# Performance work log

Hardware: AMD Instinct MI355X
Metric: run time of the kernel (lower is better)

The kernel has to match this reference:

```python
import jax, jax.numpy as jnp
import numpy as np

N_NODES = 10000
N_EDGES = 160000
N_GRAPHS = 64
X_IN = 128
HID = 64
EDGE_DIM = 16
HEADS = 4
# (in_dim, out_dim_per_head) for the 3 TransformerConv layers (concat=False)
DIMS = [(X_IN, HID), (HID, 2 * HID), (2 * HID, HID)]
WNAMES = [f"{n}{l}" for l in (1, 2, 3) for n in ("wq", "bq", "wk", "bk", "wv", "bv", "we", "ws", "bs")]


def setup_inputs() -> dict:
    key = jax.random.key(0)
    ks = iter(jax.random.split(key, 64))
    inp = {}
    inp["x"] = jax.random.normal(next(ks), (N_NODES, X_IN), jnp.float32)
    inp["edge_index"] = jax.random.randint(next(ks), (2, N_EDGES), 0, N_NODES)
    inp["edge_attr"] = jax.random.normal(next(ks), (N_EDGES, EDGE_DIM), jnp.float32)
    inp["batch"] = jnp.sort(jax.random.randint(next(ks), (N_NODES,), 0, N_GRAPHS))
    for l, (din, dout) in enumerate(DIMS, 1):
        hd = HEADS * dout
        for nm, shape in [("wq", (din, hd)), ("wk", (din, hd)), ("wv", (din, hd)),
                          ("we", (EDGE_DIM, hd)), ("ws", (din, dout))]:
            inp[f"{nm}{l}"] = jax.random.normal(next(ks), shape, jnp.float32) * 0.05
        inp[f"bq{l}"] = jnp.zeros((hd,), jnp.float32)
        inp[f"bk{l}"] = jnp.zeros((hd,), jnp.float32)
        inp[f"bv{l}"] = jnp.zeros((hd,), jnp.float32)
        inp[f"bs{l}"] = jnp.zeros((dout,), jnp.float32)
    return inp


def _transformer_conv(x, src, dst, edge_attr, wq, bq, wk, bk, wv, bv, we, ws, bs, dout):
    """PyG TransformerConv, concat=False, root_weight=True, with edge features."""
    N = x.shape[0]
    q = (x @ wq + bq).reshape(N, HEADS, dout)
    k = (x @ wk + bk).reshape(N, HEADS, dout)
    v = (x @ wv + bv).reshape(N, HEADS, dout)
    e = (edge_attr @ we).reshape(-1, HEADS, dout)  # [E, H, C]
    k_j = k[src] + e                               # edge-conditioned keys
    alpha = jnp.einsum("ehd,ehd->eh", q[dst], k_j) * (1.0 / float(dout) ** 0.5)  # [E, H]
    # numerically stable segment softmax over incoming edges of each dst node
    a_max = jax.ops.segment_max(alpha, dst, num_segments=N)
    ex = jnp.exp(alpha - a_max[dst])
    den = jax.ops.segment_sum(ex, dst, num_segments=N)
    attn = ex / den[dst]
    agg = jax.ops.segment_sum((v[src] + e) * attn[..., None], dst, num_segments=N)  # [N, H, C]
    return agg.mean(axis=1) + x @ ws + bs  # concat=False -> head mean; + skip


def _forward(x, edge_attr, edge_index, batch, params):
    src, dst = edge_index[0], edge_index[1]
    h = x
    for l, (_, dout) in enumerate(DIMS, 1):
        p = [params[f"{n}{l}"] for n in ("wq", "bq", "wk", "bk", "wv", "bv", "we", "ws", "bs")]
        h = jax.nn.elu(_transformer_conv(h, src, dst, edge_attr, *p, dout))
    # global mean pool over graphs
    s = jax.ops.segment_sum(h, batch, num_segments=N_GRAPHS)
    cnt = jax.ops.segment_sum(jnp.ones((h.shape[0], 1), h.dtype), batch, num_segments=N_GRAPHS)
    return s / jnp.maximum(cnt, 1.0)


def reference(x, edge_index, edge_attr, batch,
              wq1, bq1, wk1, bk1, wv1, bv1, we1, ws1, bs1,
              wq2, bq2, wk2, bk2, wv2, bv2, we2, ws2, bs2,
              wq3, bq3, wk3, bk3, wv3, bv3, we3, ws3, bs3):
    params = dict(locals())
    return _forward(x, edge_attr, edge_index, batch, params)
```

## Files before the change

kernel.cpp:

```cpp
#include <hip/hip_runtime.h>
#include <hip/hip_fp16.h>
#include <math.h>

#define N_NODES 10000
#define N_EDGES 160000
#define N_GRAPHS 64

using half8 = __attribute__((ext_vector_type(8))) _Float16;
using floatx4 = __attribute__((ext_vector_type(4))) float;
using h2v = __attribute__((ext_vector_type(2))) _Float16;

template <int DL> struct QW2;
template <> struct QW2<2> { using T = unsigned int; };
template <> struct QW2<4> { using T = uint2; };

__device__ inline void cvt_v(const unsigned int& w, float* dst) {
  float2 a = __half22float2(*reinterpret_cast<const __half2*>(&w));
  dst[0] = a.x; dst[1] = a.y;
}
__device__ inline void cvt_v(const uint2& w, float* dst) {
  float2 a = __half22float2(*reinterpret_cast<const __half2*>(&w.x));
  float2 b = __half22float2(*reinterpret_cast<const __half2*>(&w.y));
  dst[0] = a.x; dst[1] = a.y; dst[2] = b.x; dst[3] = b.y;
}

#if __has_builtin(__builtin_amdgcn_fdot2)
__device__ inline float dot_qk(const unsigned int& k, const unsigned int& q, float c) {
  return __builtin_amdgcn_fdot2(__builtin_bit_cast(h2v, k), __builtin_bit_cast(h2v, q), c, false);
}
__device__ inline float dot_qk(const uint2& k, const uint2& q, float c) {
  c = __builtin_amdgcn_fdot2(__builtin_bit_cast(h2v, k.x), __builtin_bit_cast(h2v, q.x), c, false);
  c = __builtin_amdgcn_fdot2(__builtin_bit_cast(h2v, k.y), __builtin_bit_cast(h2v, q.y), c, false);
  return c;
}
#else
__device__ inline float dot_qk(const unsigned int& k, const unsigned int& q, float c) {
  float kk[2], qq[2];
  cvt_v(k, kk); cvt_v(q, qq);
  return c + qq[0] * kk[0] + qq[1] * kk[1];
}
__device__ inline float dot_qk(const uint2& k, const uint2& q, float c) {
  float kk[4], qq[4];
  cvt_v(k, kk); cvt_v(q, qq);
  return c + qq[0] * kk[0] + qq[1] * kk[1] + qq[2] * kk[2] + qq[3] * kk[3];
}
#endif

__device__ inline int lower_bound(const int* b, int n, int v) {
  int lo = 0, hi = n;
  while (lo < hi) {
    int mid = (lo + hi) >> 1;
    if (b[mid] < v) lo = mid + 1; else hi = mid;
  }
  return lo;
}

template <int K, int HD, int DOUT>
__global__ __launch_bounds__(256) void gemm_mfma(
    const __half* __restrict__ A, const __half* __restrict__ Wp,
    const float* __restrict__ bias, __half* __restrict__ QS,
    __half* __restrict__ KV, int M) {
  constexpr int QSS = HD + 64 + DOUT;
  constexpr int KVS = 2 * HD;
  constexpr int KS = K / 32;
  __shared__ __half st[64][72];
  const int tid = threadIdx.x;
  const int wave = tid >> 6, lane = tid & 63;
  const int quad = lane >> 4, n16 = lane & 15;
  const int row0 = blockIdx.y * 64;
  const int col0 = blockIdx.x * 64;
  const int nblk0 = blockIdx.x * 4;

  const int arow = min(row0 + wave * 16 + n16, M - 1);
  half8 afrag[KS];
#pragma unroll
  for (int s = 0; s < KS; ++s)
    afrag[s] = *reinterpret_cast<const half8*>(A + (size_t)arow * K + s * 32 + quad * 8);

  floatx4 acc[4];
#pragma unroll
  for (int t = 0; t < 4; ++t) {
    acc[t] = (floatx4){0.f, 0.f, 0.f, 0.f};
#pragma unroll
    for (int s = 0; s < KS; ++s) {
      half8 bf = *reinterpret_cast<const half8*>(
          Wp + (((size_t)(nblk0 + t) * KS + s) * 64 + lane) * 8);
      acc[t] = __builtin_amdgcn_mfma_f32_16x16x32_f16(afrag[s], bf, acc[t], 0, 0, 0);
    }
  }

#pragma unroll
  for (int t = 0; t < 4; ++t) {
    float bv = bias[col0 + t * 16 + n16];
#pragma unroll
    for (int r = 0; r < 4; ++r)
      st[wave * 16 + quad * 4 + r][t * 16 + n16] = __float2half(acc[t][r] + bv);
  }
  __syncthreads();

  __half* dp;
  int colb, stride;
  if (col0 < HD + 64) {
    dp = QS; colb = col0; stride = QSS;
  } else if (col0 < 3 * HD + 64) {
    dp = KV; colb = col0 - HD - 64; stride = KVS;
  } else {
    dp = QS; colb = HD + 64 + (col0 - 3 * HD - 64); stride = QSS;
  }
  for (int c = tid; c < 512; c += 256) {
    int r = c >> 3, seg = c & 7;
    int row = row0 + r;
    if (row < M)
      *reinterpret_cast<uint4*>(dp + (size_t)row * stride + colb + seg * 8) =
          *reinterpret_cast<const uint4*>(&st[r][seg * 8]);
  }
}

__device__ inline void pack_layer(int i, int K, int HD, int DOUT, float scale,
                                  const float* wq, const float* wk,
                                  const float* wv, const float* wsk,
                                  const float* we, const float* bq,
                                  const float* bk, const float* bv,
                                  const float* bs, __half* Wp, float* bcat) {
  const int W = 3 * HD + DOUT + 64;
  const int KS = K / 32;
  if (i < K * W) {
    int j = i & 7, lane = (i >> 3) & 63, fs = i >> 9;
    int nblk = fs / KS, s = fs - nblk * KS;
    int quad = lane >> 4, n = lane & 15;
    int k = s * 32 + quad * 8 + j, c = nblk * 16 + n;
    float v;
    if (c < HD) {
      v = wq[k * HD + c] * scale;
    } else if (c < HD + 64) {
      int gi = c - HD, hh = gi >> 4, d = gi & 15;
      float a = 0.f;
      for (int cc = 0; cc < DOUT; ++cc)
        a += wq[k * HD + hh * DOUT + cc] * we[d * HD + hh * DOUT + cc];
      v = a * scale;
    } else if (c < 2 * HD + 64) {
      v = wk[k * HD + (c - HD - 64)];
    } else if (c < 3 * HD + 64) {
      v = wv[k * HD + (c - 2 * HD - 64)];
    } else {
      v = wsk[k * DOUT + (c - 3 * HD - 64)];
    }
    Wp[i] = __float2half(v);
  } else {
    int c = i - K * W;
    float v;
    if (c < HD) {
      v = bq[c] * scale;
    } else if (c < HD + 64) {
      int gi = c - HD, hh = gi >> 4, d = gi & 15;
      float a = 0.f;
      for (int cc = 0; cc < DOUT; ++cc)
        a += bq[hh * DOUT + cc] * we[d * HD + hh * DOUT + cc];
      v = a * scale;
    } else if (c < 2 * HD + 64) {
      v = bk[c - HD - 64];
    } else if (c < 3 * HD + 64) {
      v = bv[c - 2 * HD - 64];
    } else {
      v = bs[c - 3 * HD - 64];
    }
    bcat[c] = v;
  }
}

#define T1 115584
#define T2 227904
#define T3 343488
#define TCONV (N_NODES * 32)
#define TTOT (T3 + TCONV)
#define NZERO (2 * N_NODES + N_GRAPHS * 64)

__global__ void pack_all(
    const float* wq1, const float* wk1, const float* wv1, const float* ws1,
    const float* we1, const float* bq1, const float* bk1, const float* bv1,
    const float* bs1,
    const float* wq2, const float* wk2, const float* wv2, const float* ws2,
    const float* we2, const float* bq2, const float* bk2, const float* bv2,
    const float* bs2,
    const float* wq3, const float* wk3, const float* wv3, const float* ws3,
    const float* we3, const float* bq3, const float* bk3, const float* bv3,
    const float* bs3,
    __half* W1, float* b1, __half* W2, float* b2, __half* W3, float* b3,
    const float* x, __half* x16, int* cntz, float* doutz) {
  const float SC1 = 0.125f, SC2 = 0.08838834764831845f;
  for (int i = blockIdx.x * blockDim.x + threadIdx.x; i < NZERO;
       i += gridDim.x * blockDim.x) {
    if (i < 2 * N_NODES) cntz[i] = 0;
    else doutz[i - 2 * N_NODES] = 0.f;
  }
  for (int i = blockIdx.x * blockDim.x + threadIdx.x; i < TTOT;
       i += gridDim.x * blockDim.x) {
    if (i < T1)
      pack_layer(i, 128, 256, 64, SC1, wq1, wk1, wv1, ws1, we1, bq1, bk1, bv1, bs1, W1, b1);
    else if (i < T2)
      pack_layer(i - T1, 64, 512, 128, SC2, wq2, wk2, wv2, ws2, we2, bq2, bk2, bv2, bs2, W2, b2);
    else if (i < T3)
      pack_layer(i - T2, 128, 256, 64, SC1, wq3, wk3, wv3, ws3, we3, bq3, bk3, bv3, bs3, W3, b3);
    else {
      int k = i - T3;
      float4 v = reinterpret_cast<const float4*>(x)[k];
      __half2* o = reinterpret_cast<__half2*>(x16) + 2 * k;
      o[0] = __floats2half2_rn(v.x, v.y);
      o[1] = __floats2half2_rn(v.z, v.w);
    }
  }
}

__global__ void count_dst(const int* __restrict__ dst, int* __restrict__ cnt) {
  int e = blockIdx.x * blockDim.x + threadIdx.x;
  if (e < N_EDGES) atomicAdd(&cnt[dst[e]], 1);
}

__global__ __launch_bounds__(1024) void scan_offs(const int* __restrict__ cnt,
                                                  int* __restrict__ offs,
                                                  int* __restrict__ perm,
                                                  const int* __restrict__ batch,
                                                  float* __restrict__ invc) {
  __shared__ int part[1024];
  __shared__ int hist[256], hstart[256], hcur[256];
  const int t = threadIdx.x;
  if (t < N_GRAPHS) {
    int st = lower_bound(batch, N_NODES, t);
    int en = lower_bound(batch, N_NODES, t + 1);
    invc[t] = 1.f / (float)max(en - st, 1);
  }
  const int chunk = (N_NODES + 1023) / 1024;
  const int b = t * chunk;
  const int e = min(N_NODES, b + chunk);
  if (t < 256) { hist[t] = 0; hcur[t] = 0; }
  __syncthreads();
  int s = 0;
  for (int i = b; i < e; ++i) {
    int d = cnt[i];
    s += d;
    atomicAdd(&hist[min(d, 255)], 1);
  }
  part[t] = s;
  __syncthreads();
  for (int off = 1; off < 1024; off <<= 1) {
    int v = (t >= off) ? part[t - off] : 0;
    __syncthreads();
    part[t] += v;
    __syncthreads();
  }
  if (t == 0) {
    int acc = 0;
    for (int bk = 255; bk >= 0; --bk) { hstart[bk] = acc; acc += hist[bk]; }
    offs[N_NODES] = part[1023];
  }
  __syncthreads();
  int pre = (t == 0) ? 0 : part[t - 1];
  for (int i = b; i < e; ++i) {
    offs[i] = pre;
    int d = cnt[i];
    pre += d;
    int bkt = min(d, 255);
    int pos = hstart[bkt] + atomicAdd(&hcur[bkt], 1);
    perm[pos] = i;
  }
}

__global__ void scatter_csr(const int* __restrict__ src, const int* __restrict__ dst,
                            const float* __restrict__ edge_attr,
                            const int* __restrict__ offs, int* __restrict__ cursor,
                            int* __restrict__ csr_src, float* __restrict__ csr_ea) {
  int e = blockIdx.x * blockDim.x + threadIdx.x;
  if (e < N_EDGES) {
    int d = dst[e];
    int pos = offs[d] + atomicAdd(&cursor[d], 1);
    csr_src[pos] = src[e];
    float4* o4 = reinterpret_cast<float4*>(csr_ea + (size_t)pos * 16);
    const float4* s4 = reinterpret_cast<const float4*>(edge_attr + (size_t)e * 16);
    o4[0] = s4[0]; o4[1] = s4[1]; o4[2] = s4[2]; o4[3] = s4[3];
  }
}

template <int DOUT, bool POOL>
__global__ __launch_bounds__(128) void edge_attn(
    const __half* __restrict__ QS, const __half* __restrict__ KV,
    const float* __restrict__ we, const int* __restrict__ csr_src,
    const float* __restrict__ csr_ea, const int* __restrict__ offs,
    const int* __restrict__ perm, const int* __restrict__ batch,
    const float* __restrict__ invc, float* __restrict__ out,
    __half* __restrict__ out16) {
  constexpr int HD = 4 * DOUT;
  constexpr int QSS = HD + 64 + DOUT;
  constexpr int KVS = 2 * HD;
  constexpr int DL = DOUT / 32;
  using QT = typename QW2<DL>::T;

  __shared__ float lds[2][DOUT];

  const int tid = threadIdx.x;
  const int hp = tid >> 6;
  const int lane = tid & 63;
  const int h_local = lane >> 5;
  const int head = hp * 2 + h_local;
  const int t32 = lane & 31;
  const int c0 = t32 * DL;
  const int n = perm[blockIdx.x];

  const __half* base = QS + (size_t)n * QSS;
  QT qw = *reinterpret_cast<const QT*>(base + head * DOUT + c0);
  const float gg = (t32 < 16) ? __half2float(base[HD + head * 16 + t32]) : 0.f;
  const int eoff = t32 & 15;

  float acc[DL];
#pragma unroll
  for (int i = 0; i < DL; ++i) acc[i] = 0.f;
  float lsum = 0.f, tacc = 0.f;

  const int s0 = offs[n], s1 = offs[n + 1];
  const int kvoff = head * DOUT + c0;

  float eaA[4], eaB[4], eaC[4];
  QT krA[4], vrA[4], krB[4], vrB[4], krC[4], vrC[4];

  for (int cb = s0; cb < s1; cb += 64) {
    const int m = min(64, s1 - cb);
    const int idx = csr_src[cb + min(lane, m - 1)];
    const int ng = m >> 2;

    auto load_grp = [&](int gb, float (&ea)[4], QT (&kr)[4], QT (&vr)[4]) {
      const int bi = cb + gb;
#pragma unroll
      for (int j = 0; j < 4; ++j) ea[j] = csr_ea[(size_t)(bi + j) * 16 + eoff];
#pragma unroll
      for (int j = 0; j < 4; ++j) {
        int sj = __shfl(idx, gb + j);
        const __half* rb = KV + (size_t)sj * KVS + kvoff;
        kr[j] = *reinterpret_cast<const QT*>(rb);
        vr[j] = *reinterpret_cast<const QT*>(rb + HD);
      }
    };

    auto compute_grp = [&](float (&ea)[4], QT (&kr)[4], QT (&vr)[4]) {
      float a[4];
#pragma unroll
      for (int j = 0; j < 4; ++j) a[j] = dot_qk(kr[j], qw, ea[j] * gg);
#pragma unroll
      for (int j = 0; j < 4; ++j) {
        a[j] += __shfl_xor(a[j], 1);
        a[j] += __shfl_xor(a[j], 2);
        a[j] += __shfl_xor(a[j], 4);
        a[j] += __shfl_xor(a[j], 8);
        a[j] += __shfl_xor(a[j], 16);
      }
      float p0 = __expf(a[0]), p1 = __expf(a[1]);
      float p2 = __expf(a[2]), p3 = __expf(a[3]);
      lsum += p0 + p1 + p2 + p3;
      tacc += p0 * ea[0] + p1 * ea[1] + p2 * ea[2] + p3 * ea[3];
      float pj[4] = {p0, p1, p2, p3};
#pragma unroll
      for (int j = 0; j < 4; ++j) {
        float vv[DL];
        cvt_v(vr[j], vv);
#pragma unroll
        for (int i = 0; i < DL; ++i) acc[i] += pj[j] * vv[i];
      }
    };

    if (ng) {
      load_grp(0, eaA, krA, vrA);
      if (ng > 1) load_grp(4, eaB, krB, vrB);
      int gi = 0;
      for (;;) {
        if (gi + 2 < ng) load_grp((gi + 2) * 4, eaC, krC, vrC);
        compute_grp(eaA, krA, vrA);
        if (++gi >= ng) break;
        if (gi + 2 < ng) load_grp((gi + 2) * 4, eaA, krA, vrA);
        compute_grp(eaB, krB, vrB);
        if (++gi >= ng) break;
        if (gi + 2 < ng) load_grp((gi + 2) * 4, eaB, krB, vrB);
        compute_grp(eaC, krC, vrC);
        if (++gi >= ng) break;
      }
    }

    for (int e = ng * 4; e < m; ++e) {
      int sj = __shfl(idx, e);
      float ea0 = csr_ea[(size_t)(cb + e) * 16 + eoff];
      const __half* rb = KV + (size_t)sj * KVS + kvoff;
      QT kw = *reinterpret_cast<const QT*>(rb);
      QT vw = *reinterpret_cast<const QT*>(rb + HD);
      float a = dot_qk(kw, qw, ea0 * gg);
      a += __shfl_xor(a, 1);
      a += __shfl_xor(a, 2);
      a += __shfl_xor(a, 4);
      a += __shfl_xor(a, 8);
      a += __shfl_xor(a, 16);
      float p = __expf(a);
      lsum += p;
      tacc += p * ea0;
      float vv[DL];
      cvt_v(vw, vv);
#pragma unroll
      for (int i = 0; i < DL; ++i) acc[i] += p * vv[i];
    }
  }

  float invl = (lsum > 0.f) ? 1.f / lsum : 0.f;
  float tn = tacc * invl;
  float val[DL];
#pragma unroll
  for (int i = 0; i < DL; ++i) val[i] = acc[i] * invl;
#pragma unroll
  for (int d = 0; d < 16; ++d) {
    float td = __shfl(tn, (lane & 32) | d);
    const float* wb = we + d * HD + head * DOUT + c0;
#pragma unroll
    for (int i = 0; i < DL; ++i) val[i] += td * wb[i];
  }
#pragma unroll
  for (int i = 0; i < DL; ++i) val[i] += __shfl_xor(val[i], 32);
  if (lane < 32) {
#pragma unroll
    for (int i = 0; i < DL; ++i) lds[hp][c0 + i] = val[i];
  }
  __syncthreads();
  if (hp == 0 && lane < 32) {
    float sk[DL];
    QT sw = *reinterpret_cast<const QT*>(base + HD + 64 + c0);
    cvt_v(sw, sk);
    float o[DL];
#pragma unroll
    for (int i = 0; i < DL; ++i) {
      float tot = 0.25f * (val[i] + lds[1][c0 + i]) + sk[i];
      o[i] = (tot > 0.f) ? tot : expm1f(tot);
    }
    if (POOL) {
      int gg2 = batch[n];
      float pinv = invc[gg2];
      float* op = out + gg2 * 64 + c0;
#pragma unroll
      for (int i = 0; i < DL; ++i) atomicAdd(op + i, o[i] * pinv);
    } else {
      __half2* o16 = reinterpret_cast<__half2*>(out16 + (size_t)n * DOUT + c0);
#pragma unroll
      for (int i = 0; i < DL / 2; ++i)
        o16[i] = __floats2half2_rn(o[2 * i], o[2 * i + 1]);
    }
  }
}

extern "C" void kernel_launch(void* const* d_in, const int* in_sizes, int n_in,
                              void* d_out, int out_size, void* d_ws, size_t ws_size,
                              hipStream_t stream) {
  const float* x = (const float*)d_in[0];
  const int* edge_index = (const int*)d_in[1];
  const float* edge_attr = (const float*)d_in[2];
  const int* batch = (const int*)d_in[3];
  const int* srcp = edge_index;
  const int* dstp = edge_index + N_EDGES;

  const bool dict_order = in_sizes[5] > 1024;
  const float *wq[3], *wk[3], *wv[3], *wep[3], *wsk[3], *bq[3], *bk[3], *bv[3], *bs[3];
  for (int L = 0; L < 3; ++L) {
    int b = 4 + L * 9;
    if (dict_order) {
      wq[L] = (const float*)d_in[b + 0];
      wk[L] = (const float*)d_in[b + 1];
      wv[L] = (const float*)d_in[b + 2];
      wep[L] = (const float*)d_in[b + 3];
      wsk[L] = (const float*)d_in[b + 4];
      bq[L] = (const float*)d_in[b + 5];
      bk[L] = (const float*)d_in[b + 6];
      bv[L] = (const float*)d_in[b + 7];
      bs[L] = (const float*)d_in[b + 8];
    } else {
      wq[L] = (const float*)d_in[b + 0];
      bq[L] = (const float*)d_in[b + 1];
      wk[L] = (const float*)d_in[b + 2];
      bk[L] = (const float*)d_in[b + 3];
      wv[L] = (const float*)d_in[b + 4];
      bv[L] = (const float*)d_in[b + 5];
      wep[L] = (const float*)d_in[b + 6];
      wsk[L] = (const float*)d_in[b + 7];
      bs[L] = (const float*)d_in[b + 8];
    }
  }

  char* p = (char*)d_ws;
  __half* qs = (__half*)p;    p += (size_t)N_NODES * 704 * 2;
  __half* kv = (__half*)p;    p += (size_t)N_NODES * 1024 * 2;
  float* h1 = (float*)p;      p += (size_t)N_NODES * 64 * 4;
  __half* x16 = (__half*)p;   p += (size_t)N_NODES * 128 * 2;
  __half* h16 = (__half*)p;   p += (size_t)N_NODES * 128 * 2;
  __half* W1 = (__half*)p;    p += 128 * 896 * 2;
  __half* W2 = (__half*)p;    p += 64 * 1728 * 2;
  __half* W3 = (__half*)p;    p += 128 * 896 * 2;
  float* b1 = (float*)p;      p += 896 * 4;
  float* b2 = (float*)p;      p += 1728 * 4;
  float* b3 = (float*)p;      p += 896 * 4;
  float* invc = (float*)p;    p += 64 * 4;
  float* csr_ea = (float*)p;  p += (size_t)N_EDGES * 16 * 4;
  int* cnt = (int*)p;         p += N_NODES * 4;
  int* cursor = (int*)p;      p += N_NODES * 4;
  int* offs = (int*)p;        p += (N_NODES + 1) * 4;
  int* perm = (int*)p;        p += N_NODES * 4;
  int* csr_src = (int*)p;     p += N_EDGES * 4;

  pack_all<<<1024, 256, 0, stream>>>(
      wq[0], wk[0], wv[0], wsk[0], wep[0], bq[0], bk[0], bv[0], bs[0],
      wq[1], wk[1], wv[1], wsk[1], wep[1], bq[1], bk[1], bv[1], bs[1],
      wq[2], wk[2], wv[2], wsk[2], wep[2], bq[2], bk[2], bv[2], bs[2],
      W1, b1, W2, b2, W3, b3, x, x16, cnt, (float*)d_out);

  count_dst<<<(N_EDGES + 255) / 256, 256, 0, stream>>>(dstp, cnt);
  scan_offs<<<1, 1024, 0, stream>>>(cnt, offs, perm, batch, invc);
  scatter_csr<<<(N_EDGES + 255) / 256, 256, 0, stream>>>(srcp, dstp, edge_attr,
                                                         offs, cursor, csr_src, csr_ea);

  const int MT = (N_NODES + 63) / 64;
  gemm_mfma<128, 256, 64><<<dim3(896 / 64, MT), 256, 0, stream>>>(x16, W1, b1, qs,
                                                                  kv, N_NODES);
  edge_attn<64, false><<<N_NODES, 128, 0, stream>>>(
      qs, kv, wep[0], csr_src, csr_ea, offs, perm, batch, invc, h1, h16);
  gemm_mfma<64, 512, 128><<<dim3(1728 / 64, MT), 256, 0, stream>>>(h16, W2, b2, qs,
                                                                   kv, N_NODES);
  edge_attn<128, false><<<N_NODES, 128, 0, stream>>>(
      qs, kv, wep[1], csr_src, csr_ea, offs, perm, batch, invc, h1, h16);
  gemm_mfma<128, 256, 64><<<dim3(896 / 64, MT), 256, 0, stream>>>(h16, W3, b3, qs,
                                                                  kv, N_NODES);
  edge_attn<64, true><<<N_NODES, 128, 0, stream>>>(
      qs, kv, wep[2], csr_src, csr_ea, offs, perm, batch, invc, (float*)d_out, x16);
}
```

Baseline: 325.3 us.

## Split layer-2 edge attention per head across XCD-mapped blocks with combine pass

Replaces the layer-2 edge attention kernel with one that splits each node's work by head. Block index bits are mapped to XCDs so each XCD handles one head's K/V slice, which is meant to improve L2 locality. The inner loop is software-pipelined with a triple-buffered group prefetch and uses nontemporal loads for the CSR streams. Per-head partial results go to a new fp32 scratch buffer, and a separate combine kernel sums the heads, adds the skip term, and applies ELU. This adds extra global traffic, an extra launch, and no max-subtraction in the softmax, which risks overflow.

```diff
diff --git a/kernel.cpp b/kernel.cpp
--- a/kernel.cpp
+++ b/kernel.cpp
@@ -9,6 +9,12 @@
 using half8 = __attribute__((ext_vector_type(8))) _Float16;
 using floatx4 = __attribute__((ext_vector_type(4))) float;
 using h2v = __attribute__((ext_vector_type(2))) _Float16;
+
+#if __has_builtin(__builtin_nontemporal_load)
+#define NTLOAD(p) __builtin_nontemporal_load(p)
+#else
+#define NTLOAD(p) (*(p))
+#endif
 
 template <int DL> struct QW2;
 template <> struct QW2<2> { using T = unsigned int; };
@@ -448,6 +454,150 @@
   }
 }
 
+__global__ __launch_bounds__(128) void edge_attn2(
+    const __half* __restrict__ QS, const __half* __restrict__ KV,
+    const float* __restrict__ we, const int* __restrict__ csr_src,
+    const float* __restrict__ csr_ea, const int* __restrict__ offs,
+    const int* __restrict__ perm, float* __restrict__ hacc) {
+  const int b = blockIdx.x;
+  const int xcd = b & 7;
+  const int head = xcd >> 1;
+  const int half = xcd & 1;
+  const int w = threadIdx.x >> 6;
+  const int lane = threadIdx.x & 63;
+  const int n = perm[(b >> 3) * 4 + w * 2 + half];
+  const int le16 = lane & 15;
+  const int c0 = lane * 2;
+
+  const __half* base = QS + (size_t)n * 704;
+  const unsigned int qw =
+      *reinterpret_cast<const unsigned int*>(base + head * 128 + c0);
+  const float gg = (lane < 16) ? __half2float(base[512 + head * 16 + lane]) : 0.f;
+
+  float acc0 = 0.f, acc1 = 0.f, lsum = 0.f, tacc = 0.f;
+  const int s0 = offs[n], s1 = offs[n + 1];
+  const int kvoff = head * 128 + c0;
+
+  float eaA[4], eaB[4], eaC[4];
+  unsigned int krA[4], vrA[4], krB[4], vrB[4], krC[4], vrC[4];
+
+  for (int cb = s0; cb < s1; cb += 64) {
+    const int m = min(64, s1 - cb);
+    const int idx = NTLOAD(csr_src + cb + min(lane, m - 1));
+    const int ng = m >> 2;
+
+    auto load_grp = [&](int gb, float (&ea)[4], unsigned int (&kr)[4],
+                        unsigned int (&vr)[4]) {
+      const int bi = cb + gb;
+#pragma unroll
+      for (int j = 0; j < 4; ++j)
+        ea[j] = NTLOAD(csr_ea + (size_t)(bi + j) * 16 + le16);
+#pragma unroll
+      for (int j = 0; j < 4; ++j) {
+        int sj = __shfl(idx, gb + j);
+        const __half* rb = KV + (size_t)sj * 1024 + kvoff;
+        kr[j] = *reinterpret_cast<const unsigned int*>(rb);
+        vr[j] = *reinterpret_cast<const unsigned int*>(rb + 512);
+      }
+    };
+
+    auto compute_grp = [&](float (&ea)[4], unsigned int (&kr)[4],
+                           unsigned int (&vr)[4]) {
+      float a[4];
+#pragma unroll
+      for (int j = 0; j < 4; ++j) a[j] = dot_qk(kr[j], qw, ea[j] * gg);
+#pragma unroll
+      for (int j = 0; j < 4; ++j) {
+        a[j] += __shfl_xor(a[j], 1);
+        a[j] += __shfl_xor(a[j], 2);
+        a[j] += __shfl_xor(a[j], 4);
+        a[j] += __shfl_xor(a[j], 8);
+        a[j] += __shfl_xor(a[j], 16);
+        a[j] += __shfl_xor(a[j], 32);
+      }
+      float p0 = __expf(a[0]), p1 = __expf(a[1]);
+      float p2 = __expf(a[2]), p3 = __expf(a[3]);
+      lsum += p0 + p1 + p2 + p3;
+      tacc += p0 * ea[0] + p1 * ea[1] + p2 * ea[2] + p3 * ea[3];
+      float pj[4] = {p0, p1, p2, p3};
+#pragma unroll
+      for (int j = 0; j < 4; ++j) {
+        float vv[2];
+        cvt_v(vr[j], vv);
+        acc0 += pj[j] * vv[0];
+        acc1 += pj[j] * vv[1];
+      }
+    };
+
+    if (ng) {
+      load_grp(0, eaA, krA, vrA);
+      if (ng > 1) load_grp(4, eaB, krB, vrB);
+      int gi = 0;
+      for (;;) {
+        if (gi + 2 < ng) load_grp((gi + 2) * 4, eaC, krC, vrC);
+        compute_grp(eaA, krA, vrA);
+        if (++gi >= ng) break;
+        if (gi + 2 < ng) load_grp((gi + 2) * 4, eaA, krA, vrA);
+        compute_grp(eaB, krB, vrB);
+        if (++gi >= ng) break;
+        if (gi + 2 < ng) load_grp((gi + 2) * 4, eaB, krB, vrB);
+        compute_grp(eaC, krC, vrC);
+        if (++gi >= ng) break;
+      }
+    }
+
+    for (int e = ng * 4; e < m; ++e) {
+      int sj = __shfl(idx, e);
+      float ea0 = NTLOAD(csr_ea + (size_t)(cb + e) * 16 + le16);
+      const __half* rb = KV + (size_t)sj * 1024 + kvoff;
+      unsigned int kw = *reinterpret_cast<const unsigned int*>(rb);
+      unsigned int vw = *reinterpret_cast<const unsigned int*>(rb + 512);
+      float a = dot_qk(kw, qw, ea0 * gg);
+      a += __shfl_xor(a, 1);
+      a += __shfl_xor(a, 2);
+      a += __shfl_xor(a, 4);
+      a += __shfl_xor(a, 8);
+      a += __shfl_xor(a, 16);
+      a += __shfl_xor(a, 32);
+      float p = __expf(a);
+      lsum += p;
+      tacc += p * ea0;
+      float vv[2];
+      cvt_v(vw, vv);
+      acc0 += p * vv[0];
+      acc1 += p * vv[1];
+    }
+  }
+
+  float invl = (lsum > 0.f) ? 1.f / lsum : 0.f;
+  float tn = tacc * invl;
+  float v0 = acc0 * invl, v1 = acc1 * invl;
+#pragma unroll
+  for (int d = 0; d < 16; ++d) {
+    float td = __shfl(tn, d);
+    const float* wb = we + d * 512 + head * 128 + c0;
+    v0 += td * wb[0];
+    v1 += td * wb[1];
+  }
+  float2* hp2 = reinterpret_cast<float2*>(
+      hacc + ((size_t)head * N_NODES + n) * 128 + c0);
+  *hp2 = make_float2(0.25f * v0, 0.25f * v1);
+}
+
+__global__ __launch_bounds__(256) void combine2(
+    const float* __restrict__ hacc, const __half* __restrict__ QS,
+    __half* __restrict__ h16) {
+  int i = blockIdx.x * 256 + threadIdx.x;
+  if (i >= N_NODES * 128) return;
+  int n = i >> 7, d = i & 127;
+  const size_t NP = (size_t)N_NODES * 128;
+  float tot = hacc[i] + hacc[i + NP] + hacc[i + 2 * NP] + hacc[i + 3 * NP];
+  float sk = __half2float(QS[(size_t)n * 704 + 576 + d]);
+  float o = tot + sk;
+  o = (o > 0.f) ? o : expm1f(o);
+  h16[i] = __float2half(o);
+}
+
 extern "C" void kernel_launch(void* const* d_in, const int* in_sizes, int n_in,
                               void* d_out, int out_size, void* d_ws, size_t ws_size,
                               hipStream_t stream) {
@@ -504,6 +654,7 @@
   int* offs = (int*)p;        p += (N_NODES + 1) * 4;
   int* perm = (int*)p;        p += N_NODES * 4;
   int* csr_src = (int*)p;     p += N_EDGES * 4;
+  float* hacc = (float*)p;    p += (size_t)4 * N_NODES * 128 * 4;
 
   pack_all<<<1024, 256, 0, stream>>>(
       wq[0], wk[0], wv[0], wsk[0], wep[0], bq[0], bk[0], bv[0], bs[0],
@@ -523,8 +674,9 @@
       qs, kv, wep[0], csr_src, csr_ea, offs, perm, batch, invc, h1, h16);
   gemm_mfma<64, 512, 128><<<dim3(1728 / 64, MT), 256, 0, stream>>>(h16, W2, b2, qs,
                                                                    kv, N_NODES);
-  edge_attn<128, false><<<N_NODES, 128, 0, stream>>>(
-      qs, kv, wep[1], csr_src, csr_ea, offs, perm, batch, invc, h1, h16);
+  edge_attn2<<<N_NODES * 2, 128, 0, stream>>>(qs, kv, wep[1], csr_src, csr_ea,
+                                              offs, perm, hacc);
+  combine2<<<(N_NODES * 128 + 255) / 256, 256, 0, stream>>>(hacc, qs, h16);
   gemm_mfma<128, 256, 64><<<dim3(896 / 64, MT), 256, 0, stream>>>(h16, W3, b3, qs,
                                                                   kv, N_NODES);
   edge_attn<64, true><<<N_NODES, 128, 0, stream>>>(
```

Result: slower. 350.5 us (+7.7%).
